# Kernel optimization log

Hardware: AMD Instinct MI355X
Metric: run time of the kernel (lower is better)

The kernel has to match this reference:

```python
import jax, jax.numpy as jnp
import numpy as np

B, T, F, H = 4096, 48, 64, 128


def _uniform(key, shape, stdv):
    return jax.random.uniform(key, shape, jnp.float32, -stdv, stdv)


def setup_inputs() -> dict:
    key = jax.random.key(0)
    ks = jax.random.split(key, 24)
    values = jax.random.normal(ks[0], (B, T, F), jnp.float32)
    masks = (jax.random.uniform(ks[1], (B, T, F)) < 0.8).astype(jnp.float32)
    deltas = jax.random.uniform(ks[2], (B, T, F), jnp.float32)
    sH = 1.0 / np.sqrt(H)
    sF = 1.0 / np.sqrt(F)
    inp = {
        "values": values, "masks": masks, "deltas": deltas,
        # TemporalDecay h: W [H, F], b [H] (stdv = 1/sqrt(out=H))
        "Wdh": _uniform(ks[3], (H, F), sH), "bdh": _uniform(ks[4], (H,), sH),
        # TemporalDecay x (diag): W [F, F], b [F]
        "Wdx": _uniform(ks[5], (F, F), sF), "bdx": _uniform(ks[6], (F,), sF),
        # hist_reg: Linear(H -> F)
        "Wh": _uniform(ks[7], (F, H), sH), "bh": _uniform(ks[8], (F,), sH),
        # feat_reg: masked F x F
        "Wf": _uniform(ks[9], (F, F), sF), "bf": _uniform(ks[10], (F,), sF),
        # weight_combine: Linear(2F -> F)
        "Wc": _uniform(ks[11], (F, 2 * F), 1.0 / np.sqrt(2 * F)),
        "bc": _uniform(ks[12], (F,), 1.0 / np.sqrt(2 * F)),
        # LSTMCell(2F -> H): gates in PyTorch order i, f, g, o
        "W_ih": _uniform(ks[13], (4 * H, 2 * F), sH),
        "W_hh": _uniform(ks[14], (4 * H, H), sH),
        "b_ih": _uniform(ks[15], (4 * H,), sH),
        "b_hh": _uniform(ks[16], (4 * H,), sH),
        # out: Linear(H -> 1)
        "Wo": _uniform(ks[17], (1, H), sH), "bo": _uniform(ks[18], (1,), sH),
    }
    return inp


def reference(values, masks, deltas, Wdh, bdh, Wdx, bdx, Wh, bh, Wf, bf,
              Wc, bc, W_ih, W_hh, b_ih, b_hh, Wo, bo):
    impute_weight = 1.0
    b, t, f = values.shape
    h_dim = Wdh.shape[0]
    eye = jnp.eye(f, dtype=values.dtype)
    Wdx_m = Wdx * eye            # diagonal temporal decay
    Wf_m = Wf * (1.0 - eye)

    def step(carry, xt):
        h, c, loss = carry
        x, m, d = xt  # each [B, F]
        gamma_h = jnp.exp(-jax.nn.relu(d @ Wdh.T + bdh))        # [B, H]
        gamma_x = jnp.exp(-jax.nn.relu(d @ Wdx_m.T + bdx))      # [B, F]
        h = h * gamma_h
        x_h = h @ Wh.T + bh
        denom = jnp.sum(m) + 1e-5
        loss = loss + jnp.sum(jnp.abs(x - x_h) * m) / denom
        x_c = m * x + (1.0 - m) * x_h
        z_h = x_c @ Wf_m.T + bf
        loss = loss + jnp.sum(jnp.abs(x - z_h) * m) / denom
        alpha = jnp.concatenate([gamma_x, m], axis=1) @ Wc.T + bc
        c_h = alpha * z_h + (1.0 - alpha) * x_h
        loss = loss + jnp.sum(jnp.abs(x - c_h) * m) / denom
        c_c = m * x + (1.0 - m) * c_h
        inputs = jnp.concatenate([c_c, m], axis=1)  # [B, 2F]
        gates = inputs @ W_ih.T + b_ih + h @ W_hh.T + b_hh
        i_g, f_g, g_g, o_g = jnp.split(gates, 4, axis=1)
        c = jax.nn.sigmoid(f_g) * c + jax.nn.sigmoid(i_g) * jnp.tanh(g_g)
        h = jax.nn.sigmoid(o_g) * jnp.tanh(c)
        return (h, c, loss), c_c

    init = (jnp.zeros((b, h_dim), values.dtype),
            jnp.zeros((b, h_dim), values.dtype),
            jnp.zeros((), values.dtype))
    xs = (jnp.swapaxes(values, 0, 1),
          jnp.swapaxes(masks, 0, 1),
          jnp.swapaxes(deltas, 0, 1))
    (h, c, x_loss), imps = jax.lax.scan(step, init, xs)
    imputations = jnp.swapaxes(imps, 0, 1)  # [B, T, F]
    predictions = h @ Wo.T + bo             # [B, 1]
    return x_loss * impute_weight, imputations, predictions
```

## Files before the change

kernel.cpp:

```cpp
#include <hip/hip_runtime.h>
#include <hip/hip_bf16.h>
#include <math.h>

#define BB 4096
#define TT 48
#define FF 64
#define HH 128
#define ROWS 16
#define NT 512
#define NBLK (BB / ROWS)

typedef __attribute__((ext_vector_type(8))) short short8;
typedef __attribute__((ext_vector_type(4))) float f32x4;

#define MFMA(a, b, c) __builtin_amdgcn_mfma_f32_16x16x32_bf16((a), (b), (c), 0, 0, 0)

__device__ __forceinline__ float sigm(float x) { return 1.f / (1.f + __expf(-x)); }
__device__ __forceinline__ float tanh_f(float x) { return 2.f / (1.f + __expf(-2.f * x)) - 1.f; }

__global__ __launch_bounds__(256) void prep_kernel(
    const float* __restrict__ W_ih, const float* __restrict__ W_hh,
    const float* __restrict__ Wdh,  const float* __restrict__ Wh,
    const float* __restrict__ Wf,   const float* __restrict__ Wc,
    __hip_bfloat16* __restrict__ frags) {
    const int idx = blockIdx.x * 256 + threadIdx.x;
    float v;
    if (idx < 131072) {
        const int jj = idx & 7;
        const int lane = (idx >> 3) & 63;
        const int ks = (idx >> 9) & 7;
        const int tile = idx >> 12;
        const int n = tile * 16 + (lane & 15);
        const int k = ks * 32 + ((lane >> 4) << 3) + jj;
        v = (k < 128) ? W_ih[n * 128 + k] : W_hh[n * 128 + (k - 128)];
    } else {
        const int u = idx - 131072;
        const int jj = u & 7;
        const int lane = (u >> 3) & 63;
        const int lq = lane & 15, q8 = (lane >> 4) << 3;
        if (u < 8192) {
            const int ks = (u >> 9) & 1, nt = u >> 10;
            const int n = nt * 16 + lq, k = ks * 32 + q8 + jj;
            v = Wdh[n * 64 + k];
        } else if (u < 16384) {
            const int uu = u - 8192;
            const int ks = (uu >> 9) & 3, nt = uu >> 11;
            const int n = nt * 16 + lq, k = ks * 32 + q8 + jj;
            v = Wh[n * 128 + k];
        } else if (u < 20480) {
            const int uu = u - 16384;
            const int ks = (uu >> 9) & 1, nt = uu >> 10;
            const int n = nt * 16 + lq, k = ks * 32 + q8 + jj;
            v = (k == n) ? 0.f : Wf[n * 64 + k];
        } else {
            const int uu = u - 20480;
            const int ks = (uu >> 9) & 3, nt = uu >> 11;
            const int n = nt * 16 + lq, k = ks * 32 + q8 + jj;
            v = Wc[n * 128 + k];
        }
    }
    frags[idx] = __float2bfloat16(v);
}

__global__ __launch_bounds__(256) void denom1_kernel(const float* __restrict__ masks,
                                                     float* __restrict__ partials) {
    const int t = blockIdx.x >> 5;
    const int s = blockIdx.x & 31;
    const int tid = threadIdx.x;
    float acc = 0.f;
    #pragma unroll
    for (int k = 0; k < 8; ++k) {
        const int i = k * 256 + tid;
        const int b = s * 128 + (i >> 4);
        const int f = (i & 15) << 2;
        const float4 v = *(const float4*)&masks[((size_t)b * TT + t) * FF + f];
        acc += v.x + v.y + v.z + v.w;
    }
    #pragma unroll
    for (int off = 32; off; off >>= 1) acc += __shfl_down(acc, off, 64);
    __shared__ float red[4];
    if ((tid & 63) == 0) red[tid >> 6] = acc;
    __syncthreads();
    if (tid == 0) partials[blockIdx.x] = red[0] + red[1] + red[2] + red[3];
}

__global__ __launch_bounds__(64) void denom2_kernel(const float* __restrict__ partials,
                                                    float* __restrict__ inv_denom) {
    const int t = threadIdx.x;
    if (t < TT) {
        float s = 0.f;
        #pragma unroll
        for (int i = 0; i < 32; ++i) s += partials[t * 32 + i];
        inv_denom[t] = 1.f / (s + 1e-5f);
    }
}

__global__ __launch_bounds__(NT, 2) void rits_kernel(
    const float* __restrict__ values, const float* __restrict__ masks,
    const float* __restrict__ deltas,
    const float* __restrict__ Wdx, const float* __restrict__ bdx,
    const float* __restrict__ bdh, const float* __restrict__ bh,
    const float* __restrict__ bf,  const float* __restrict__ bc,
    const float* __restrict__ b_ih, const float* __restrict__ b_hh,
    const float* __restrict__ Wo,  const float* __restrict__ bo,
    const __hip_bfloat16* __restrict__ frags,
    const float* __restrict__ inv_denom,
    float* __restrict__ ws_lossblk,
    float* __restrict__ out_imp, float* __restrict__ out_pred)
{
    __shared__ short8 whh_frag[8192];
    __shared__ __hip_bfloat16 dbuf[ROWS][72];
    __shared__ __hip_bfloat16 gxbuf[ROWS][72];
    __shared__ __hip_bfloat16 mbuf[ROWS][72];
    __shared__ __hip_bfloat16 xcbuf[ROWS][72];
    __shared__ __hip_bfloat16 ccbuf[ROWS][72];
    __shared__ __hip_bfloat16 hbufB[ROWS][136];
    __shared__ float x_lds[ROWS][65];
    __shared__ float m_lds[ROWS][65];
    __shared__ float redl[8];

    const int tid = threadIdx.x;
    const int bid = blockIdx.x;
    const int b0 = bid * ROWS;
    const int lane = tid & 63;
    const int wv = tid >> 6;
    const int quad = lane >> 4;
    const int lq = lane & 15;
    const int wv3 = wv & 3;

    const float wdx_l = Wdx[lane * (FF + 1)];
    const float bdx_l = bdx[lane];

    const int j_ln = wv * 16 + lq;
    const float bdh_w = bdh[j_ln];
    const float bI = b_ih[j_ln]       + b_hh[j_ln];
    const float bF = b_ih[128 + j_ln] + b_hh[128 + j_ln];
    const float bG = b_ih[256 + j_ln] + b_hh[256 + j_ln];
    const float bO = b_ih[384 + j_ln] + b_hh[384 + j_ln];

    const int f46 = wv3 * 16 + lq;
    const float bh_f = bh[f46];
    const float bf_f = bf[f46];
    const float bc_f = bc[f46];

    const short8* f8 = (const short8*)frags;

    short8 Bgam[2], Bal[4], Bxh[4], Bzh[2];
    #pragma unroll
    for (int ks = 0; ks < 2; ++ks) Bgam[ks] = f8[16384 + ((wv * 2 + ks) << 6) + lane];
    #pragma unroll
    for (int ks = 0; ks < 4; ++ks) Bal[ks] = f8[18944 + ((wv3 * 4 + ks) << 6) + lane];
    #pragma unroll
    for (int ks = 0; ks < 4; ++ks) Bxh[ks] = f8[17408 + ((wv3 * 4 + ks) << 6) + lane];
    #pragma unroll
    for (int ks = 0; ks < 2; ++ks) Bzh[ks] = f8[18432 + ((wv3 * 2 + ks) << 6) + lane];

    short8 Bcc[4][2], Bm[4][2];
    #pragma unroll
    for (int g = 0; g < 4; ++g) {
        #pragma unroll
        for (int kk = 0; kk < 2; ++kk) {
            Bcc[g][kk] = f8[(((g * 8 + wv) * 8 + kk)     << 6) + lane];
            Bm[g][kk]  = f8[(((g * 8 + wv) * 8 + 2 + kk) << 6) + lane];
        }
    }
    for (int i = tid; i < 8192; i += NT) {
        const int slot = i >> 6, ln = i & 63;
        const int g = slot >> 5, rem = slot & 31, j = rem >> 2, kk = rem & 3;
        whh_frag[i] = f8[(((g * 8 + j) * 8 + 4 + kk) << 6) + ln];
    }
    const int wbase = (wv << 8) + lane;

    float c_reg[4], h_reg[4];
    #pragma unroll
    for (int r = 0; r < 4; ++r) { c_reg[r] = 0.f; h_reg[r] = 0.f; }
    float loss_acc = 0.f;

    const int base0 = ((b0 + wv) * TT) * FF + lane;
    const int base1 = ((b0 + wv + 8) * TT) * FF + lane;
    const int imp0  = ((b0 + quad * 4) * TT) * FF + f46;

    float xn0 = values[base0], mn0 = masks[base0], dn0 = deltas[base0];
    float xn1 = values[base1], mn1 = masks[base1], dn1 = deltas[base1];
    {
        const int r0 = wv, r1 = wv + 8;
        x_lds[r0][lane] = xn0; m_lds[r0][lane] = mn0;
        dbuf[r0][lane]  = __float2bfloat16(dn0);
        gxbuf[r0][lane] = __float2bfloat16(__expf(-fmaxf(fmaf(dn0, wdx_l, bdx_l), 0.f)));
        mbuf[r0][lane]  = __float2bfloat16(mn0);
        x_lds[r1][lane] = xn1; m_lds[r1][lane] = mn1;
        dbuf[r1][lane]  = __float2bfloat16(dn1);
        gxbuf[r1][lane] = __float2bfloat16(__expf(-fmaxf(fmaf(dn1, wdx_l, bdx_l), 0.f)));
        mbuf[r1][lane]  = __float2bfloat16(mn1);
    }
    __syncthreads();

    for (int t = 0; t < TT; ++t) {
        const float invd = inv_denom[t];

        {
            const int tn = (t < TT - 1) ? t + 1 : t;
            const int o0 = base0 + tn * FF, o1 = base1 + tn * FF;
            xn0 = values[o0]; mn0 = masks[o0]; dn0 = deltas[o0];
            xn1 = values[o1]; mn1 = masks[o1]; dn1 = deltas[o1];
        }
        f32x4 gacc0 = {0.f,0.f,0.f,0.f}, gacc1 = {0.f,0.f,0.f,0.f};
        f32x4 gacc2 = {0.f,0.f,0.f,0.f}, gacc3 = {0.f,0.f,0.f,0.f};
        #pragma unroll
        for (int kk = 0; kk < 2; ++kk) {
            const short8 a = *(const short8*)&mbuf[lq][kk * 32 + quad * 8];
            gacc0 = MFMA(a, Bm[0][kk], gacc0);
            gacc1 = MFMA(a, Bm[1][kk], gacc1);
            gacc2 = MFMA(a, Bm[2][kk], gacc2);
            gacc3 = MFMA(a, Bm[3][kk], gacc3);
        }
        float al_r[4];
        {
            f32x4 ga = {0.f, 0.f, 0.f, 0.f};
            #pragma unroll
            for (int ks = 0; ks < 2; ++ks) {
                const short8 a = *(const short8*)&dbuf[lq][ks * 32 + quad * 8];
                ga = MFMA(a, Bgam[ks], ga);
            }
            if (wv < 4) {
                f32x4 aa = {0.f, 0.f, 0.f, 0.f};
                #pragma unroll
                for (int ks = 0; ks < 2; ++ks) {
                    const short8 a = *(const short8*)&gxbuf[lq][ks * 32 + quad * 8];
                    aa = MFMA(a, Bal[ks], aa);
                }
                #pragma unroll
                for (int ks = 2; ks < 4; ++ks) {
                    const short8 a = *(const short8*)&mbuf[lq][(ks - 2) * 32 + quad * 8];
                    aa = MFMA(a, Bal[ks], aa);
                }
                #pragma unroll
                for (int r = 0; r < 4; ++r) al_r[r] = aa[r] + bc_f;
            }
            #pragma unroll
            for (int r = 0; r < 4; ++r) {
                const float gh = __expf(-fmaxf(ga[r] + bdh_w, 0.f));
                hbufB[quad * 4 + r][j_ln] = __float2bfloat16(h_reg[r] * gh);
            }
        }
        __syncthreads();

        #pragma unroll
        for (int kk = 0; kk < 2; ++kk) {
            const short8 a = *(const short8*)&hbufB[lq][kk * 32 + quad * 8];
            gacc0 = MFMA(a, whh_frag[wbase + 0    + kk * 64], gacc0);
            gacc1 = MFMA(a, whh_frag[wbase + 2048 + kk * 64], gacc1);
            gacc2 = MFMA(a, whh_frag[wbase + 4096 + kk * 64], gacc2);
            gacc3 = MFMA(a, whh_frag[wbase + 6144 + kk * 64], gacc3);
        }
        float xv_r[4], mv_r[4], xh_r[4];
        float stepsum = 0.f;
        if (wv < 4) {
            f32x4 acc = {0.f, 0.f, 0.f, 0.f};
            #pragma unroll
            for (int ks = 0; ks < 4; ++ks) {
                const short8 a = *(const short8*)&hbufB[lq][ks * 32 + quad * 8];
                acc = MFMA(a, Bxh[ks], acc);
            }
            #pragma unroll
            for (int r = 0; r < 4; ++r) {
                const int row = quad * 4 + r;
                const float xh = acc[r] + bh_f;
                xh_r[r] = xh;
                const float xv = x_lds[row][f46], mv = m_lds[row][f46];
                xv_r[r] = xv; mv_r[r] = mv;
                stepsum += mv * fabsf(xv - xh);
                xcbuf[row][f46] = __float2bfloat16(fmaf(mv, xv, (1.f - mv) * xh));
            }
        }
        __syncthreads();

        #pragma unroll
        for (int kk = 2; kk < 4; ++kk) {
            const short8 a = *(const short8*)&hbufB[lq][kk * 32 + quad * 8];
            gacc0 = MFMA(a, whh_frag[wbase + 0    + kk * 64], gacc0);
            gacc1 = MFMA(a, whh_frag[wbase + 2048 + kk * 64], gacc1);
            gacc2 = MFMA(a, whh_frag[wbase + 4096 + kk * 64], gacc2);
            gacc3 = MFMA(a, whh_frag[wbase + 6144 + kk * 64], gacc3);
        }
        if (wv < 4) {
            f32x4 acc5 = {0.f, 0.f, 0.f, 0.f};
            #pragma unroll
            for (int ks = 0; ks < 2; ++ks) {
                const short8 a = *(const short8*)&xcbuf[lq][ks * 32 + quad * 8];
                acc5 = MFMA(a, Bzh[ks], acc5);
            }
            #pragma unroll
            for (int r = 0; r < 4; ++r) {
                const int row = quad * 4 + r;
                const float zh = acc5[r] + bf_f;
                stepsum += mv_r[r] * fabsf(xv_r[r] - zh);
                const float alpha = al_r[r];
                const float ch = fmaf(alpha, zh, (1.f - alpha) * xh_r[r]);
                stepsum += mv_r[r] * fabsf(xv_r[r] - ch);
                const float cc = fmaf(mv_r[r], xv_r[r], (1.f - mv_r[r]) * ch);
                ccbuf[row][f46] = __float2bfloat16(cc);
                out_imp[imp0 + r * (TT * FF) + t * FF] = cc;
            }
        }
        loss_acc = fmaf(stepsum, invd, loss_acc);
        __syncthreads();

        #pragma unroll
        for (int kk = 0; kk < 2; ++kk) {
            const short8 a = *(const short8*)&ccbuf[lq][kk * 32 + quad * 8];
            gacc0 = MFMA(a, Bcc[0][kk], gacc0);
            gacc1 = MFMA(a, Bcc[1][kk], gacc1);
            gacc2 = MFMA(a, Bcc[2][kk], gacc2);
            gacc3 = MFMA(a, Bcc[3][kk], gacc3);
        }
        {
            const int r0 = wv, r1 = wv + 8;
            x_lds[r0][lane] = xn0; m_lds[r0][lane] = mn0;
            dbuf[r0][lane]  = __float2bfloat16(dn0);
            gxbuf[r0][lane] = __float2bfloat16(__expf(-fmaxf(fmaf(dn0, wdx_l, bdx_l), 0.f)));
            mbuf[r0][lane]  = __float2bfloat16(mn0);
            x_lds[r1][lane] = xn1; m_lds[r1][lane] = mn1;
            dbuf[r1][lane]  = __float2bfloat16(dn1);
            gxbuf[r1][lane] = __float2bfloat16(__expf(-fmaxf(fmaf(dn1, wdx_l, bdx_l), 0.f)));
            mbuf[r1][lane]  = __float2bfloat16(mn1);
        }
        #pragma unroll
        for (int r = 0; r < 4; ++r) {
            const float ig = sigm(gacc0[r] + bI);
            const float fg = sigm(gacc1[r] + bF);
            const float gg = tanh_f(gacc2[r] + bG);
            const float og = sigm(gacc3[r] + bO);
            c_reg[r] = fmaf(fg, c_reg[r], ig * gg);
            h_reg[r] = og * tanh_f(c_reg[r]);
        }
        __syncthreads();
    }

    #pragma unroll
    for (int r = 0; r < 4; ++r)
        hbufB[quad * 4 + r][j_ln] = __float2bfloat16(h_reg[r]);
    __syncthreads();
    {
        const int r = tid >> 5, l = tid & 31;
        float s = 0.f;
        #pragma unroll
        for (int k = l; k < HH; k += 32) s += __bfloat162float(hbufB[r][k]) * Wo[k];
        #pragma unroll
        for (int off = 16; off; off >>= 1) s += __shfl_down(s, off, 32);
        if (l == 0) out_pred[b0 + r] = s + bo[0];
    }
    #pragma unroll
    for (int off = 32; off; off >>= 1) loss_acc += __shfl_down(loss_acc, off, 64);
    if (lane == 0) redl[wv] = loss_acc;
    __syncthreads();
    if (tid == 0) {
        float s = 0.f;
        #pragma unroll
        for (int w = 0; w < 8; ++w) s += redl[w];
        ws_lossblk[bid] = s;
    }
}

__global__ __launch_bounds__(256) void final_kernel(const float* __restrict__ ws_lossblk,
                                                    float* __restrict__ out_loss) {
    const int tid = threadIdx.x;
    float s = ws_lossblk[tid];
    #pragma unroll
    for (int off = 32; off; off >>= 1) s += __shfl_down(s, off, 64);
    __shared__ float red[4];
    if ((tid & 63) == 0) red[tid >> 6] = s;
    __syncthreads();
    if (tid == 0) out_loss[0] = red[0] + red[1] + red[2] + red[3];
}

extern "C" void kernel_launch(void* const* d_in, const int* in_sizes, int n_in,
                              void* d_out, int out_size, void* d_ws, size_t ws_size,
                              hipStream_t stream) {
    const float* values = (const float*)d_in[0];
    const float* masks  = (const float*)d_in[1];
    const float* deltas = (const float*)d_in[2];
    const float* Wdh  = (const float*)d_in[3];
    const float* bdh  = (const float*)d_in[4];
    const float* Wdx  = (const float*)d_in[5];
    const float* bdx  = (const float*)d_in[6];
    const float* Wh   = (const float*)d_in[7];
    const float* bh   = (const float*)d_in[8];
    const float* Wf   = (const float*)d_in[9];
    const float* bf   = (const float*)d_in[10];
    const float* Wc   = (const float*)d_in[11];
    const float* bc   = (const float*)d_in[12];
    const float* W_ih = (const float*)d_in[13];
    const float* W_hh = (const float*)d_in[14];
    const float* b_ih = (const float*)d_in[15];
    const float* b_hh = (const float*)d_in[16];
    const float* Wo   = (const float*)d_in[17];
    const float* bo   = (const float*)d_in[18];

    __hip_bfloat16* frags = (__hip_bfloat16*)d_ws;
    float* inv_denom  = (float*)((char*)d_ws + 320 * 1024);
    float* partials   = inv_denom + 64;
    float* ws_lossblk = partials + 2048;

    float* out_loss = (float*)d_out;
    float* out_imp  = out_loss + 1;
    float* out_pred = out_imp + (size_t)BB * TT * FF;

    prep_kernel<<<624, 256, 0, stream>>>(W_ih, W_hh, Wdh, Wh, Wf, Wc, frags);
    denom1_kernel<<<TT * 32, 256, 0, stream>>>(masks, partials);
    denom2_kernel<<<1, 64, 0, stream>>>(partials, inv_denom);
    rits_kernel<<<NBLK, NT, 0, stream>>>(
        values, masks, deltas, Wdx, bdx, bdh, bh, bf, bc,
        b_ih, b_hh, Wo, bo, frags, inv_denom, ws_lossblk, out_imp, out_pred);
    final_kernel<<<1, 256, 0, stream>>>(ws_lossblk, out_loss);
}
```

Before: 318.4 us.

## Compute next-step hidden decay at step end to drop a barrier per step

The gamma_h decay of the hidden state for the next timestep is now computed at the end of the current step, right after the LSTM update, and the decayed h is written to the shared buffer there. The next step can start the W_hh and x_h MFMAs immediately, so one __syncthreads per timestep is removed and the recurrent matmul is issued in one block. The deltas buffer write moves earlier in the step, and the hidden-state buffer is zero-initialised to cover the first step. This adds some work to the tail of each step and depends on careful ordering of the shared-memory buffer updates.

```diff
diff --git a/kernel.cpp b/kernel.cpp
--- a/kernel.cpp
+++ b/kernel.cpp
@@ -180,16 +180,15 @@
     const int base1 = ((b0 + wv + 8) * TT) * FF + lane;
     const int imp0  = ((b0 + quad * 4) * TT) * FF + f46;
 
+    for (int i = tid; i < ROWS * 136; i += NT) ((unsigned short*)hbufB)[i] = 0;
     float xn0 = values[base0], mn0 = masks[base0], dn0 = deltas[base0];
     float xn1 = values[base1], mn1 = masks[base1], dn1 = deltas[base1];
     {
         const int r0 = wv, r1 = wv + 8;
         x_lds[r0][lane] = xn0; m_lds[r0][lane] = mn0;
-        dbuf[r0][lane]  = __float2bfloat16(dn0);
         gxbuf[r0][lane] = __float2bfloat16(__expf(-fmaxf(fmaf(dn0, wdx_l, bdx_l), 0.f)));
         mbuf[r0][lane]  = __float2bfloat16(mn0);
         x_lds[r1][lane] = xn1; m_lds[r1][lane] = mn1;
-        dbuf[r1][lane]  = __float2bfloat16(dn1);
         gxbuf[r1][lane] = __float2bfloat16(__expf(-fmaxf(fmaf(dn1, wdx_l, bdx_l), 0.f)));
         mbuf[r1][lane]  = __float2bfloat16(mn1);
     }
@@ -204,8 +203,59 @@
             xn0 = values[o0]; mn0 = masks[o0]; dn0 = deltas[o0];
             xn1 = values[o1]; mn1 = masks[o1]; dn1 = deltas[o1];
         }
+        f32x4 xacc = {0.f,0.f,0.f,0.f}, aa = {0.f,0.f,0.f,0.f};
+        if (wv < 4) {
+            #pragma unroll
+            for (int ks = 0; ks < 4; ++ks) {
+                const short8 a = *(const short8*)&hbufB[lq][ks * 32 + quad * 8];
+                xacc = MFMA(a, Bxh[ks], xacc);
+            }
+            #pragma unroll
+            for (int ks = 0; ks < 2; ++ks) {
+                const short8 a = *(const short8*)&gxbuf[lq][ks * 32 + quad * 8];
+                aa = MFMA(a, Bal[ks], aa);
+            }
+            #pragma unroll
+            for (int ks = 2; ks < 4; ++ks) {
+                const short8 a = *(const short8*)&mbuf[lq][(ks - 2) * 32 + quad * 8];
+                aa = MFMA(a, Bal[ks], aa);
+            }
+        }
         f32x4 gacc0 = {0.f,0.f,0.f,0.f}, gacc1 = {0.f,0.f,0.f,0.f};
         f32x4 gacc2 = {0.f,0.f,0.f,0.f}, gacc3 = {0.f,0.f,0.f,0.f};
+        #pragma unroll
+        for (int kk = 0; kk < 4; ++kk) {
+            const short8 a = *(const short8*)&hbufB[lq][kk * 32 + quad * 8];
+            gacc0 = MFMA(a, whh_frag[wbase + 0    + kk * 64], gacc0);
+            gacc1 = MFMA(a, whh_frag[wbase + 2048 + kk * 64], gacc1);
+            gacc2 = MFMA(a, whh_frag[wbase + 4096 + kk * 64], gacc2);
+            gacc3 = MFMA(a, whh_frag[wbase + 6144 + kk * 64], gacc3);
+        }
+        float al_r[4], xv_r[4], mv_r[4], xh_r[4];
+        float stepsum = 0.f;
+        if (wv < 4) {
+            #pragma unroll
+            for (int r = 0; r < 4; ++r) {
+                al_r[r] = aa[r] + bc_f;
+                const int row = quad * 4 + r;
+                const float xh = xacc[r] + bh_f;
+                xh_r[r] = xh;
+                const float xv = x_lds[row][f46], mv = m_lds[row][f46];
+                xv_r[r] = xv; mv_r[r] = mv;
+                stepsum += mv * fabsf(xv - xh);
+                xcbuf[row][f46] = __float2bfloat16(fmaf(mv, xv, (1.f - mv) * xh));
+            }
+        }
+        __syncthreads();
+
+        f32x4 acc5 = {0.f,0.f,0.f,0.f};
+        if (wv < 4) {
+            #pragma unroll
+            for (int ks = 0; ks < 2; ++ks) {
+                const short8 a = *(const short8*)&xcbuf[lq][ks * 32 + quad * 8];
+                acc5 = MFMA(a, Bzh[ks], acc5);
+            }
+        }
         #pragma unroll
         for (int kk = 0; kk < 2; ++kk) {
             const short8 a = *(const short8*)&mbuf[lq][kk * 32 + quad * 8];
@@ -214,82 +264,9 @@
             gacc2 = MFMA(a, Bm[2][kk], gacc2);
             gacc3 = MFMA(a, Bm[3][kk], gacc3);
         }
-        float al_r[4];
-        {
-            f32x4 ga = {0.f, 0.f, 0.f, 0.f};
-            #pragma unroll
-            for (int ks = 0; ks < 2; ++ks) {
-                const short8 a = *(const short8*)&dbuf[lq][ks * 32 + quad * 8];
-                ga = MFMA(a, Bgam[ks], ga);
-            }
-            if (wv < 4) {
-                f32x4 aa = {0.f, 0.f, 0.f, 0.f};
-                #pragma unroll
-                for (int ks = 0; ks < 2; ++ks) {
-                    const short8 a = *(const short8*)&gxbuf[lq][ks * 32 + quad * 8];
-                    aa = MFMA(a, Bal[ks], aa);
-                }
-                #pragma unroll
-                for (int ks = 2; ks < 4; ++ks) {
-                    const short8 a = *(const short8*)&mbuf[lq][(ks - 2) * 32 + quad * 8];
-                    aa = MFMA(a, Bal[ks], aa);
-                }
-                #pragma unroll
-                for (int r = 0; r < 4; ++r) al_r[r] = aa[r] + bc_f;
-            }
-            #pragma unroll
-            for (int r = 0; r < 4; ++r) {
-                const float gh = __expf(-fmaxf(ga[r] + bdh_w, 0.f));
-                hbufB[quad * 4 + r][j_ln] = __float2bfloat16(h_reg[r] * gh);
-            }
-        }
-        __syncthreads();
-
-        #pragma unroll
-        for (int kk = 0; kk < 2; ++kk) {
-            const short8 a = *(const short8*)&hbufB[lq][kk * 32 + quad * 8];
-            gacc0 = MFMA(a, whh_frag[wbase + 0    + kk * 64], gacc0);
-            gacc1 = MFMA(a, whh_frag[wbase + 2048 + kk * 64], gacc1);
-            gacc2 = MFMA(a, whh_frag[wbase + 4096 + kk * 64], gacc2);
-            gacc3 = MFMA(a, whh_frag[wbase + 6144 + kk * 64], gacc3);
-        }
-        float xv_r[4], mv_r[4], xh_r[4];
-        float stepsum = 0.f;
+        dbuf[wv][lane]     = __float2bfloat16(dn0);
+        dbuf[wv + 8][lane] = __float2bfloat16(dn1);
         if (wv < 4) {
-            f32x4 acc = {0.f, 0.f, 0.f, 0.f};
-            #pragma unroll
-            for (int ks = 0; ks < 4; ++ks) {
-                const short8 a = *(const short8*)&hbufB[lq][ks * 32 + quad * 8];
-                acc = MFMA(a, Bxh[ks], acc);
-            }
-            #pragma unroll
-            for (int r = 0; r < 4; ++r) {
-                const int row = quad * 4 + r;
-                const float xh = acc[r] + bh_f;
-                xh_r[r] = xh;
-                const float xv = x_lds[row][f46], mv = m_lds[row][f46];
-                xv_r[r] = xv; mv_r[r] = mv;
-                stepsum += mv * fabsf(xv - xh);
-                xcbuf[row][f46] = __float2bfloat16(fmaf(mv, xv, (1.f - mv) * xh));
-            }
-        }
-        __syncthreads();
-
-        #pragma unroll
-        for (int kk = 2; kk < 4; ++kk) {
-            const short8 a = *(const short8*)&hbufB[lq][kk * 32 + quad * 8];
-            gacc0 = MFMA(a, whh_frag[wbase + 0    + kk * 64], gacc0);
-            gacc1 = MFMA(a, whh_frag[wbase + 2048 + kk * 64], gacc1);
-            gacc2 = MFMA(a, whh_frag[wbase + 4096 + kk * 64], gacc2);
-            gacc3 = MFMA(a, whh_frag[wbase + 6144 + kk * 64], gacc3);
-        }
-        if (wv < 4) {
-            f32x4 acc5 = {0.f, 0.f, 0.f, 0.f};
-            #pragma unroll
-            for (int ks = 0; ks < 2; ++ks) {
-                const short8 a = *(const short8*)&xcbuf[lq][ks * 32 + quad * 8];
-                acc5 = MFMA(a, Bzh[ks], acc5);
-            }
             #pragma unroll
             for (int r = 0; r < 4; ++r) {
                 const int row = quad * 4 + r;
@@ -306,6 +283,12 @@
         loss_acc = fmaf(stepsum, invd, loss_acc);
         __syncthreads();
 
+        f32x4 ga = {0.f,0.f,0.f,0.f};
+        #pragma unroll
+        for (int ks = 0; ks < 2; ++ks) {
+            const short8 a = *(const short8*)&dbuf[lq][ks * 32 + quad * 8];
+            ga = MFMA(a, Bgam[ks], ga);
+        }
         #pragma unroll
         for (int kk = 0; kk < 2; ++kk) {
             const short8 a = *(const short8*)&ccbuf[lq][kk * 32 + quad * 8];
@@ -317,11 +300,9 @@
         {
             const int r0 = wv, r1 = wv + 8;
             x_lds[r0][lane] = xn0; m_lds[r0][lane] = mn0;
-            dbuf[r0][lane]  = __float2bfloat16(dn0);
             gxbuf[r0][lane] = __float2bfloat16(__expf(-fmaxf(fmaf(dn0, wdx_l, bdx_l), 0.f)));
             mbuf[r0][lane]  = __float2bfloat16(mn0);
             x_lds[r1][lane] = xn1; m_lds[r1][lane] = mn1;
-            dbuf[r1][lane]  = __float2bfloat16(dn1);
             gxbuf[r1][lane] = __float2bfloat16(__expf(-fmaxf(fmaf(dn1, wdx_l, bdx_l), 0.f)));
             mbuf[r1][lane]  = __float2bfloat16(mn1);
         }
@@ -333,6 +314,8 @@
             const float og = sigm(gacc3[r] + bO);
             c_reg[r] = fmaf(fg, c_reg[r], ig * gg);
             h_reg[r] = og * tanh_f(c_reg[r]);
+            const float gh = __expf(-fmaxf(ga[r] + bdh_w, 0.f));
+            hbufB[quad * 4 + r][j_ln] = __float2bfloat16(h_reg[r] * gh);
         }
         __syncthreads();
     }
```

Measured after the change: 326.1 us. +2.4%, slower.
